# Performance work log

Hardware: AMD Instinct MI355X
Metric: run time of the kernel (lower is better)

## Reference

```python
import jax, jax.numpy as jnp
import numpy as np

B, T, S = 64, 100, 1024
IN, SRC, TRG = 256, 256, 512
ENC = 2 * SRC  # bidirectional encoder hidden width


def setup_inputs() -> dict:
    key = jax.random.key(0)
    ks = jax.random.split(key, 16)
    n = lambda k, shape, sc: jax.random.normal(k, shape, jnp.float32) * sc
    return {
        "idx": 0,
        "input_": n(ks[0], (B, T, IN), 1.0),
        "h0": n(ks[1], (B, TRG), 1.0),
        "c0": n(ks[2], (B, TRG), 1.0),
        "h_attn": jnp.zeros((B, TRG), jnp.float32),
        "encoder_hy": n(ks[3], (B, S, ENC), 1.0),
        "past_attn": jnp.zeros((B, S), jnp.float32),
        "past_dehy": jnp.zeros((B, 1, TRG), jnp.float32),
        # LSTMCell params (PyTorch layout, gate order i,f,g,o)
        "w_ih": n(ks[4], (4 * TRG, IN + TRG), 0.05),
        "b_ih": jnp.zeros((4 * TRG,), jnp.float32),
        "w_hh": n(ks[5], (4 * TRG, TRG), 0.05),
        "b_hh": jnp.zeros((4 * TRG,), jnp.float32),
        # AttentionEncoder luong_concat params
        "w_en": n(ks[6], (TRG, ENC), 0.05),
        "b_en": jnp.zeros((TRG,), jnp.float32),
        "w_de": n(ks[7], (TRG, TRG), 0.05),
        "w_cv": n(ks[8], (TRG, 1), 0.05),
        "w_warp": n(ks[9], (1, TRG), 0.05),
        # attn_out: Linear(ENC + TRG, TRG)
        "w_ao": n(ks[10], (TRG, ENC + TRG), 0.05),
        "b_ao": jnp.zeros((TRG,), jnp.float32),
        # pt_out: Linear(IN + ENC + TRG, 1)
        "w_pt": n(ks[11], (1, IN + ENC + TRG), 0.05),
        "b_pt": jnp.zeros((1,), jnp.float32),
    }


def reference(idx, input_, h0, c0, h_attn, encoder_hy, past_attn, past_dehy,
              w_ih, b_ih, w_hh, b_hh, w_en, b_en, w_de, w_cv, w_warp,
              w_ao, b_ao, w_pt, b_pt):
    # Config: lstm, luong_concat attention, repetition='asee' (coverage),
    # pointer_net=True, attn_decoder=False.
    enc_proj = jnp.einsum('bse,he->bsh', encoder_hy, w_en) + b_en  # hoisted W_en*enhy, [B,S,TRG]
    cv_w = w_cv[:, 0]      # [TRG]
    warp_w = w_warp[0]     # [TRG]
    xs = jnp.swapaxes(input_, 0, 1)  # [T,B,IN]

    def step(carry, x_t):
        h, c, ha, pa = carry
        # LSTMCell on cat(x_t, h_attn)
        x = jnp.concatenate([x_t, ha], axis=1)
        gates = x @ w_ih.T + b_ih + h @ w_hh.T + b_hh
        i, f, g, o = jnp.split(gates, 4, axis=1)
        c_new = jax.nn.sigmoid(f) * c + jax.nn.sigmoid(i) * jnp.tanh(g)
        h_new = jax.nn.sigmoid(o) * jnp.tanh(c_new)
        # luong_concat score with asee coverage term
        agg = jnp.tanh(enc_proj + (h_new @ w_de.T)[:, None, :] + pa[:, :, None] * cv_w)
        attn_ee = jnp.einsum('bsh,h->bs', agg, warp_w)
        attn = jax.nn.softmax(attn_ee, axis=1)
        c_enc = jnp.einsum('bs,bse->be', attn, encoder_hy)  # encoder context
        ha_new = jnp.concatenate([c_enc, h_new], axis=1) @ w_ao.T + b_ao
        pa_new = pa + attn  # coverage accumulation (repetition 'asee')
        p = jax.nn.sigmoid(jnp.concatenate([x_t, h_new, c_enc], axis=1) @ w_pt.T + b_pt)[:, 0]
        return (h_new, c_new, ha_new, pa_new), (ha_new, attn, p)

    (hT, cT, haT, paT), (outs, attns, pgens) = jax.lax.scan(
        step, (h0, c0, h_attn, past_attn), xs)
    output_ = jnp.swapaxes(outs, 0, 1)   # [B,T,TRG]
    p_gen = jnp.swapaxes(pgens, 0, 1)    # [B,T]
    loss_cv = jnp.zeros((1,), jnp.float32)  # only nonzero for 'asee_train'
    # matches original return signature; out_attn kept [T,B,S] as in source
    return (output_, (hT, cT), haT, attns, paT, p_gen, past_dehy, loss_cv)
```

## Files before the change

### kernel.cpp

```cpp
#include <hip/hip_runtime.h>
#include <stdint.h>

typedef __attribute__((ext_vector_type(8))) short short8;
typedef __attribute__((ext_vector_type(4))) float f32x4;

#define DEV static __device__ __forceinline__

DEV unsigned short f2bf(float f) {
  union { float f; uint32_t u; } v; v.f = f;
  uint32_t r = (v.u + 0x7fffu + ((v.u >> 16) & 1u)) >> 16;
  return (unsigned short)r;
}
DEV float bf2f(unsigned short h) {
  union { uint32_t u; float f; } v; v.u = ((uint32_t)h) << 16;
  return v.f;
}
DEV float fsigmoid(float x) { return 1.f / (1.f + __expf(-x)); }
DEV float ftanh(float x) {
  float e = __expf(2.f * x);
  return 1.f - 2.f / (e + 1.f);
}

static const size_t O_HT    = 3276800;
static const size_t O_CT    = 3309568;
static const size_t O_HAT   = 3342336;
static const size_t O_ATTNS = 3375104;
static const size_t O_PAT   = 9928704;
static const size_t O_PGEN  = 9994240;
static const size_t O_PDEHY = 10000640;
static const size_t O_LOSS  = 10033408;

__global__ __launch_bounds__(256) void k_conv_bf16(const float* __restrict__ in,
                                                   unsigned short* __restrict__ out) {
  size_t i = (size_t)blockIdx.x * blockDim.x + threadIdx.x;
  f32x4 v = ((const f32x4*)in)[i];
  uint32_t lo = (uint32_t)f2bf(v[0]) | ((uint32_t)f2bf(v[1]) << 16);
  uint32_t hi = (uint32_t)f2bf(v[2]) | ((uint32_t)f2bf(v[3]) << 16);
  ((uint2*)out)[i] = make_uint2(lo, hi);
}

__global__ __launch_bounds__(256) void k_build_wcomb(const float* __restrict__ wih,
                                                     const float* __restrict__ whh,
                                                     unsigned short* __restrict__ wc) {
  int i = blockIdx.x * blockDim.x + threadIdx.x;
  int base = i * 4;
  int n = base / 1280, k = base - n * 1280;
  const float* src = (k < 768) ? (wih + (size_t)n * 768 + k) : (whh + (size_t)n * 512 + (k - 768));
  f32x4 v = *(const f32x4*)src;
  uint32_t lo = (uint32_t)f2bf(v[0]) | ((uint32_t)f2bf(v[1]) << 16);
  uint32_t hi = (uint32_t)f2bf(v[2]) | ((uint32_t)f2bf(v[3]) << 16);
  ((uint2*)wc)[i] = make_uint2(lo, hi);
}

__global__ __launch_bounds__(256) void k_bias(const float* __restrict__ a,
                                              const float* __restrict__ b,
                                              float* __restrict__ o) {
  int i = blockIdx.x * blockDim.x + threadIdx.x;
  o[i] = a[i] + b[i];
}

template <int MT, int NT, int KK, int OUTBF>
__global__ __launch_bounds__(256) void k_gemm_bt(const unsigned short* __restrict__ A,
                                                 const unsigned short* __restrict__ Bm,
                                                 const float* __restrict__ bias,
                                                 void* __restrict__ C, int ldc) {
  int wid = (int)((blockIdx.x * blockDim.x + threadIdx.x) >> 6);
  int lane = threadIdx.x & 63;
  int tm = wid % MT, tn = wid / MT;
  int r = lane & 15, q = lane >> 4;
  const short8* Ap = (const short8*)(A + (size_t)(tm * 16 + r) * KK + q * 8);
  const short8* Bp = (const short8*)(Bm + (size_t)(tn * 16 + r) * KK + q * 8);
  f32x4 acc = {0.f, 0.f, 0.f, 0.f};
#pragma unroll 4
  for (int kk = 0; kk < KK / 32; ++kk) {
    acc = __builtin_amdgcn_mfma_f32_16x16x32_bf16(Ap[kk * 4], Bp[kk * 4], acc, 0, 0, 0);
  }
  int col = tn * 16 + r;
  float bv = bias ? bias[col] : 0.f;
#pragma unroll
  for (int rg = 0; rg < 4; ++rg) {
    int row = tm * 16 + q * 4 + rg;
    float v = acc[rg] + bv;
    if (OUTBF) ((unsigned short*)C)[(size_t)row * ldc + col] = f2bf(v);
    else       ((float*)C)[(size_t)row * ldc + col] = v;
  }
}

__global__ __launch_bounds__(256) void k_gemm_ha(const float* __restrict__ cenc,
                                                 const unsigned short* __restrict__ hb,
                                                 const unsigned short* __restrict__ Bm,
                                                 const float* __restrict__ bias,
                                                 float* __restrict__ out) {
  int wid = (int)((blockIdx.x * blockDim.x + threadIdx.x) >> 6);
  int lane = threadIdx.x & 63;
  int tm = wid & 3, tn = wid >> 2;
  int r = lane & 15, q = lane >> 4;
  int arow = tm * 16 + r;
  f32x4 acc = {0.f, 0.f, 0.f, 0.f};
#pragma unroll
  for (int kk = 0; kk < 32; ++kk) {
    int k0 = kk * 32 + q * 8;
    short8 a;
    if (k0 < 512) {
      const f32x4* p = (const f32x4*)(cenc + (size_t)arow * 512 + k0);
      f32x4 lo = p[0], hi = p[1];
#pragma unroll
      for (int j = 0; j < 4; ++j) { a[j] = (short)f2bf(lo[j]); a[4 + j] = (short)f2bf(hi[j]); }
    } else {
      a = *(const short8*)(hb + (size_t)arow * 512 + (k0 - 512));
    }
    short8 b = *(const short8*)(Bm + (size_t)(tn * 16 + r) * 1024 + k0);
    acc = __builtin_amdgcn_mfma_f32_16x16x32_bf16(a, b, acc, 0, 0, 0);
  }
  int col = tn * 16 + r;
  float bv = bias[col];
#pragma unroll
  for (int rg = 0; rg < 4; ++rg) {
    int row = tm * 16 + q * 4 + rg;
    out[(size_t)row * 512 + col] = acc[rg] + bv;
  }
}

__global__ __launch_bounds__(256) void k_pack(const float* __restrict__ input_,
                                              const float* __restrict__ ha,
                                              const float* __restrict__ h,
                                              unsigned short* __restrict__ xf, int t) {
  int idx = blockIdx.x * blockDim.x + threadIdx.x;
  int b = idx / 1280, k = idx - b * 1280;
  float v;
  if (k < 256)      v = input_[((size_t)b * 100 + t) * 256 + k];
  else if (k < 768) v = ha[b * 512 + (k - 256)];
  else              v = h[b * 512 + (k - 768)];
  xf[idx] = f2bf(v);
}

__global__ __launch_bounds__(256) void k_lstm(const float* __restrict__ gates,
                                              float* __restrict__ h, float* __restrict__ c,
                                              unsigned short* __restrict__ hb) {
  int idx = blockIdx.x * blockDim.x + threadIdx.x;
  int b = idx >> 9, n = idx & 511;
  const float* g = gates + (size_t)b * 2048;
  float iv = fsigmoid(g[n]);
  float fv = fsigmoid(g[512 + n]);
  float gv = ftanh(g[1024 + n]);
  float ov = fsigmoid(g[1536 + n]);
  float cn = fv * c[idx] + iv * gv;
  float hn = ov * ftanh(cn);
  c[idx] = cn; h[idx] = hn; hb[idx] = f2bf(hn);
}

__global__ __launch_bounds__(256) void k_attn_ee(const unsigned short* __restrict__ ep,
                                                 const float* __restrict__ de,
                                                 const float* __restrict__ cv,
                                                 const float* __restrict__ wwarp,
                                                 const float* __restrict__ pa,
                                                 float* __restrict__ ee) {
  int wid = (int)((blockIdx.x * blockDim.x + threadIdx.x) >> 6);
  int lane = threadIdx.x & 63;
  int b = wid >> 10, s = wid & 1023;
  float pav = pa[(size_t)b * 1024 + s];
  short8 v = *(const short8*)(ep + ((size_t)b * 1024 + s) * 512 + lane * 8);
  const f32x4* dp = (const f32x4*)(de + b * 512 + lane * 8);
  f32x4 d0 = dp[0], d1 = dp[1];
  const f32x4* cp = (const f32x4*)(cv + lane * 8);
  f32x4 c0 = cp[0], c1 = cp[1];
  const f32x4* wp = (const f32x4*)(wwarp + lane * 8);
  f32x4 w0 = wp[0], w1 = wp[1];
  float acc = 0.f;
#pragma unroll
  for (int j = 0; j < 4; ++j) {
    float x0 = bf2f((unsigned short)v[j]) + d0[j] + pav * c0[j];
    acc += ftanh(x0) * w0[j];
    float x1 = bf2f((unsigned short)v[4 + j]) + d1[j] + pav * c1[j];
    acc += ftanh(x1) * w1[j];
  }
#pragma unroll
  for (int off = 32; off > 0; off >>= 1) acc += __shfl_xor(acc, off, 64);
  if (lane == 0) ee[(size_t)b * 1024 + s] = acc;
}

__global__ __launch_bounds__(256) void k_softmax(const float* __restrict__ ee,
                                                 float* __restrict__ attn,
                                                 float* __restrict__ attns_out,
                                                 float* __restrict__ pa,
                                                 float* __restrict__ cenc) {
  int b = blockIdx.x, tid = threadIdx.x;
  int wv = tid >> 6, lane = tid & 63;
  __shared__ float red[4];
  f32x4 v = ((const f32x4*)(ee + (size_t)b * 1024))[tid];
  float m = fmaxf(fmaxf(v[0], v[1]), fmaxf(v[2], v[3]));
#pragma unroll
  for (int off = 32; off > 0; off >>= 1) m = fmaxf(m, __shfl_xor(m, off, 64));
  if (lane == 0) red[wv] = m;
  __syncthreads();
  m = fmaxf(fmaxf(red[0], red[1]), fmaxf(red[2], red[3]));
  f32x4 e;
  e[0] = __expf(v[0] - m); e[1] = __expf(v[1] - m);
  e[2] = __expf(v[2] - m); e[3] = __expf(v[3] - m);
  float s = e[0] + e[1] + e[2] + e[3];
#pragma unroll
  for (int off = 32; off > 0; off >>= 1) s += __shfl_xor(s, off, 64);
  __syncthreads();
  if (lane == 0) red[wv] = s;
  __syncthreads();
  s = red[0] + red[1] + red[2] + red[3];
  float inv = 1.f / s;
  f32x4 a;
  a[0] = e[0] * inv; a[1] = e[1] * inv; a[2] = e[2] * inv; a[3] = e[3] * inv;
  ((f32x4*)(attn + (size_t)b * 1024))[tid] = a;
  ((f32x4*)(attns_out + (size_t)b * 1024))[tid] = a;
  f32x4* pap = (f32x4*)(pa + (size_t)b * 1024);
  f32x4 p = pap[tid];
  p[0] += a[0]; p[1] += a[1]; p[2] += a[2]; p[3] += a[3];
  pap[tid] = p;
  cenc[(size_t)b * 512 + tid] = 0.f;
  cenc[(size_t)b * 512 + 256 + tid] = 0.f;
}

__global__ __launch_bounds__(256) void k_cenc(const float* __restrict__ attn,
                                              const unsigned short* __restrict__ encb,
                                              float* __restrict__ cenc) {
  int b = blockIdx.x >> 2, sq = blockIdx.x & 3;
  int e0 = threadIdx.x * 2;
  const float* at = attn + (size_t)b * 1024 + sq * 256;
  const uint32_t* ep = (const uint32_t*)(encb + ((size_t)b * 1024 + sq * 256) * 512 + e0);
  float a0 = 0.f, a1 = 0.f;
#pragma unroll 4
  for (int s = 0; s < 256; ++s) {
    float w = at[s];
    uint32_t pk = ep[(size_t)s * 256];
    a0 += w * bf2f((unsigned short)(pk & 0xffffu));
    a1 += w * bf2f((unsigned short)(pk >> 16));
  }
  atomicAdd(&cenc[(size_t)b * 512 + e0], a0);
  atomicAdd(&cenc[(size_t)b * 512 + e0 + 1], a1);
}

__global__ __launch_bounds__(256) void k_pout(const float* __restrict__ input_,
                                              const float* __restrict__ h,
                                              const float* __restrict__ c,
                                              const float* __restrict__ cenc,
                                              const float* __restrict__ ha,
                                              const float* __restrict__ wpt,
                                              const float* __restrict__ bpt,
                                              float* __restrict__ dout, int t) {
  int b = blockIdx.x, tid = threadIdx.x;
  float acc = 0.f;
#pragma unroll
  for (int k = tid; k < 1280; k += 256) {
    float x;
    if (k < 256)      x = input_[((size_t)b * 100 + t) * 256 + k];
    else if (k < 768) x = h[(size_t)b * 512 + (k - 256)];
    else              x = cenc[(size_t)b * 512 + (k - 768)];
    acc += x * wpt[k];
  }
  int wv = tid >> 6, lane = tid & 63;
  __shared__ float red[4];
#pragma unroll
  for (int off = 32; off > 0; off >>= 1) acc += __shfl_xor(acc, off, 64);
  if (lane == 0) red[wv] = acc;
  __syncthreads();
  if (tid == 0) {
    float p = fsigmoid(red[0] + red[1] + red[2] + red[3] + bpt[0]);
    dout[O_PGEN + (size_t)b * 100 + t] = p;
  }
  float v0 = ha[(size_t)b * 512 + tid];
  float v1 = ha[(size_t)b * 512 + 256 + tid];
  dout[((size_t)b * 100 + t) * 512 + tid] = v0;
  dout[((size_t)b * 100 + t) * 512 + 256 + tid] = v1;
  if (t == 99) {
    dout[O_HT  + (size_t)b * 512 + tid]       = h[(size_t)b * 512 + tid];
    dout[O_HT  + (size_t)b * 512 + 256 + tid] = h[(size_t)b * 512 + 256 + tid];
    dout[O_CT  + (size_t)b * 512 + tid]       = c[(size_t)b * 512 + tid];
    dout[O_CT  + (size_t)b * 512 + 256 + tid] = c[(size_t)b * 512 + 256 + tid];
    dout[O_HAT + (size_t)b * 512 + tid]       = v0;
    dout[O_HAT + (size_t)b * 512 + 256 + tid] = v1;
  }
}

extern "C" void kernel_launch(void* const* d_in, const int* in_sizes, int n_in,
                              void* d_out, int out_size, void* d_ws, size_t ws_size,
                              hipStream_t stream) {
  const float* input_    = (const float*)d_in[1];
  const float* h0        = (const float*)d_in[2];
  const float* c0        = (const float*)d_in[3];
  const float* h_attn    = (const float*)d_in[4];
  const float* encoder_hy= (const float*)d_in[5];
  const float* past_attn = (const float*)d_in[6];
  const float* past_dehy = (const float*)d_in[7];
  const float* w_ih      = (const float*)d_in[8];
  const float* b_ih      = (const float*)d_in[9];
  const float* w_hh      = (const float*)d_in[10];
  const float* b_hh      = (const float*)d_in[11];
  const float* w_en      = (const float*)d_in[12];
  const float* b_en      = (const float*)d_in[13];
  const float* w_de      = (const float*)d_in[14];
  const float* w_cv      = (const float*)d_in[15];
  const float* w_warp    = (const float*)d_in[16];
  const float* w_ao      = (const float*)d_in[17];
  const float* b_ao      = (const float*)d_in[18];
  const float* w_pt      = (const float*)d_in[19];
  const float* b_pt      = (const float*)d_in[20];

  char* ws = (char*)d_ws;
  unsigned short* encb  = (unsigned short*)(ws + 0);
  unsigned short* epb   = (unsigned short*)(ws + 67108864);
  unsigned short* wcomb = (unsigned short*)(ws + 134217728);
  unsigned short* wenb  = (unsigned short*)(ws + 139460608);
  unsigned short* wdeb  = (unsigned short*)(ws + 139984896);
  unsigned short* waob  = (unsigned short*)(ws + 140509184);
  float* biasc          = (float*)(ws + 141557760);
  unsigned short* xf    = (unsigned short*)(ws + 141565952);
  float* gates          = (float*)(ws + 141729792);
  float* h              = (float*)(ws + 142254080);
  float* c              = (float*)(ws + 142385152);
  float* ha             = (float*)(ws + 142516224);
  unsigned short* hb    = (unsigned short*)(ws + 142647296);
  float* de             = (float*)(ws + 142712832);
  float* ee             = (float*)(ws + 142843904);
  float* attn           = (float*)(ws + 143106048);
  float* cenc           = (float*)(ws + 143368192);

  float* out = (float*)d_out;
  float* pa = out + O_PAT;

  hipMemcpyAsync(h,  h0,     32768 * 4, hipMemcpyDeviceToDevice, stream);
  hipMemcpyAsync(c,  c0,     32768 * 4, hipMemcpyDeviceToDevice, stream);
  hipMemcpyAsync(ha, h_attn, 32768 * 4, hipMemcpyDeviceToDevice, stream);
  hipMemcpyAsync(pa, past_attn, 65536 * 4, hipMemcpyDeviceToDevice, stream);
  hipMemcpyAsync(out + O_PDEHY, past_dehy, 32768 * 4, hipMemcpyDeviceToDevice, stream);
  hipMemsetAsync(out + O_LOSS, 0, 4, stream);

  k_conv_bf16<<<32768, 256, 0, stream>>>(encoder_hy, encb);
  k_conv_bf16<<<256, 256, 0, stream>>>(w_en, wenb);
  k_conv_bf16<<<256, 256, 0, stream>>>(w_de, wdeb);
  k_conv_bf16<<<512, 256, 0, stream>>>(w_ao, waob);
  k_build_wcomb<<<2560, 256, 0, stream>>>(w_ih, w_hh, wcomb);
  k_bias<<<8, 256, 0, stream>>>(b_ih, b_hh, biasc);

  k_gemm_bt<4096, 32, 512, 1><<<32768, 256, 0, stream>>>(encb, wenb, b_en, epb, 512);

  for (int t = 0; t < 100; ++t) {
    k_pack<<<320, 256, 0, stream>>>(input_, ha, h, xf, t);
    k_gemm_bt<4, 128, 1280, 0><<<128, 256, 0, stream>>>(xf, wcomb, biasc, gates, 2048);
    k_lstm<<<128, 256, 0, stream>>>(gates, h, c, hb);
    k_gemm_bt<4, 32, 512, 0><<<32, 256, 0, stream>>>(hb, wdeb, nullptr, de, 512);
    k_attn_ee<<<16384, 256, 0, stream>>>(epb, de, w_cv, w_warp, pa, ee);
    k_softmax<<<64, 256, 0, stream>>>(ee, attn, out + O_ATTNS + (size_t)t * 65536, pa, cenc);
    k_cenc<<<256, 256, 0, stream>>>(attn, encb, cenc);
    k_gemm_ha<<<32, 256, 0, stream>>>(cenc, hb, waob, b_ao, ha);
    k_pout<<<64, 256, 0, stream>>>(input_, h, c, cenc, ha, w_pt, b_pt, out, t);
  }
}
```

Baseline: 8.984 ms.

## Fuse per-step kernels: gates+LSTM, softmax+context, attn-out+pointer

Per-step launches drop from nine to five. Packing, the gate GEMM and the LSTM cell become one kernel that reads fp32 inputs and converts them to bf16 inline. Each wave computes all four gate tiles for its columns, and h's bf16 copy is double-buffered. Softmax and context accumulation merge into one 1024-thread block per batch using shared-memory partials instead of atomics, and the ha GEMM runs as a block-split kernel alongside the pointer-gate reduction. The intent is to cut launch overhead and intermediate global traffic. In exchange, the gate GEMM runs on only 32 blocks and the context step has only 64 blocks.

```diff
diff --git a/kernel.cpp b/kernel.cpp
--- a/kernel.cpp
+++ b/kernel.cpp
@@ -19,6 +19,12 @@
 DEV float ftanh(float x) {
   float e = __expf(2.f * x);
   return 1.f - 2.f / (e + 1.f);
+}
+DEV short8 pack_bf16x8(f32x4 lo, f32x4 hi) {
+  short8 a;
+#pragma unroll
+  for (int j = 0; j < 4; ++j) { a[j] = (short)f2bf(lo[j]); a[4 + j] = (short)f2bf(hi[j]); }
+  return a;
 }
 
 static const size_t O_HT    = 3276800;
@@ -86,67 +92,56 @@
   }
 }
 
-__global__ __launch_bounds__(256) void k_gemm_ha(const float* __restrict__ cenc,
-                                                 const unsigned short* __restrict__ hb,
-                                                 const unsigned short* __restrict__ Bm,
-                                                 const float* __restrict__ bias,
-                                                 float* __restrict__ out) {
-  int wid = (int)((blockIdx.x * blockDim.x + threadIdx.x) >> 6);
-  int lane = threadIdx.x & 63;
-  int tm = wid & 3, tn = wid >> 2;
+__global__ __launch_bounds__(256) void k_gates_lstm(
+    const float* __restrict__ input_, const float* __restrict__ ha,
+    const unsigned short* __restrict__ hbp,
+    const unsigned short* __restrict__ wcomb,
+    const float* __restrict__ biasc,
+    float* __restrict__ h, float* __restrict__ c,
+    unsigned short* __restrict__ hbn,
+    int t) {
+  int wave = threadIdx.x >> 6, lane = threadIdx.x & 63;
   int r = lane & 15, q = lane >> 4;
-  int arow = tm * 16 + r;
-  f32x4 acc = {0.f, 0.f, 0.f, 0.f};
-#pragma unroll
-  for (int kk = 0; kk < 32; ++kk) {
+  int ns = blockIdx.x;
+  int arow = wave * 16 + r;
+  int bcol = ns * 16 + r;
+  const unsigned short* B0 = wcomb + (size_t)(bcol) * 1280;
+  const unsigned short* B1 = wcomb + (size_t)(512 + bcol) * 1280;
+  const unsigned short* B2 = wcomb + (size_t)(1024 + bcol) * 1280;
+  const unsigned short* B3 = wcomb + (size_t)(1536 + bcol) * 1280;
+  f32x4 acc0 = {0.f,0.f,0.f,0.f}, acc1 = acc0, acc2 = acc0, acc3 = acc0;
+#pragma unroll 4
+  for (int kk = 0; kk < 40; ++kk) {
     int k0 = kk * 32 + q * 8;
     short8 a;
-    if (k0 < 512) {
-      const f32x4* p = (const f32x4*)(cenc + (size_t)arow * 512 + k0);
-      f32x4 lo = p[0], hi = p[1];
-#pragma unroll
-      for (int j = 0; j < 4; ++j) { a[j] = (short)f2bf(lo[j]); a[4 + j] = (short)f2bf(hi[j]); }
+    if (k0 < 256) {
+      const f32x4* p = (const f32x4*)(input_ + ((size_t)arow * 100 + t) * 256 + k0);
+      a = pack_bf16x8(p[0], p[1]);
+    } else if (k0 < 768) {
+      const f32x4* p = (const f32x4*)(ha + (size_t)arow * 512 + (k0 - 256));
+      a = pack_bf16x8(p[0], p[1]);
     } else {
-      a = *(const short8*)(hb + (size_t)arow * 512 + (k0 - 512));
-    }
-    short8 b = *(const short8*)(Bm + (size_t)(tn * 16 + r) * 1024 + k0);
-    acc = __builtin_amdgcn_mfma_f32_16x16x32_bf16(a, b, acc, 0, 0, 0);
-  }
-  int col = tn * 16 + r;
-  float bv = bias[col];
+      a = *(const short8*)(hbp + (size_t)arow * 512 + (k0 - 768));
+    }
+    acc0 = __builtin_amdgcn_mfma_f32_16x16x32_bf16(a, *(const short8*)(B0 + k0), acc0, 0, 0, 0);
+    acc1 = __builtin_amdgcn_mfma_f32_16x16x32_bf16(a, *(const short8*)(B1 + k0), acc1, 0, 0, 0);
+    acc2 = __builtin_amdgcn_mfma_f32_16x16x32_bf16(a, *(const short8*)(B2 + k0), acc2, 0, 0, 0);
+    acc3 = __builtin_amdgcn_mfma_f32_16x16x32_bf16(a, *(const short8*)(B3 + k0), acc3, 0, 0, 0);
+  }
+  int col = ns * 16 + r;
+  float bi = biasc[col], bf = biasc[512 + col], bg = biasc[1024 + col], bo = biasc[1536 + col];
 #pragma unroll
   for (int rg = 0; rg < 4; ++rg) {
-    int row = tm * 16 + q * 4 + rg;
-    out[(size_t)row * 512 + col] = acc[rg] + bv;
-  }
-}
-
-__global__ __launch_bounds__(256) void k_pack(const float* __restrict__ input_,
-                                              const float* __restrict__ ha,
-                                              const float* __restrict__ h,
-                                              unsigned short* __restrict__ xf, int t) {
-  int idx = blockIdx.x * blockDim.x + threadIdx.x;
-  int b = idx / 1280, k = idx - b * 1280;
-  float v;
-  if (k < 256)      v = input_[((size_t)b * 100 + t) * 256 + k];
-  else if (k < 768) v = ha[b * 512 + (k - 256)];
-  else              v = h[b * 512 + (k - 768)];
-  xf[idx] = f2bf(v);
-}
-
-__global__ __launch_bounds__(256) void k_lstm(const float* __restrict__ gates,
-                                              float* __restrict__ h, float* __restrict__ c,
-                                              unsigned short* __restrict__ hb) {
-  int idx = blockIdx.x * blockDim.x + threadIdx.x;
-  int b = idx >> 9, n = idx & 511;
-  const float* g = gates + (size_t)b * 2048;
-  float iv = fsigmoid(g[n]);
-  float fv = fsigmoid(g[512 + n]);
-  float gv = ftanh(g[1024 + n]);
-  float ov = fsigmoid(g[1536 + n]);
-  float cn = fv * c[idx] + iv * gv;
-  float hn = ov * ftanh(cn);
-  c[idx] = cn; h[idx] = hn; hb[idx] = f2bf(hn);
+    int b = wave * 16 + q * 4 + rg;
+    size_t idx = (size_t)b * 512 + col;
+    float iv = fsigmoid(acc0[rg] + bi);
+    float fv = fsigmoid(acc1[rg] + bf);
+    float gv = ftanh(acc2[rg] + bg);
+    float ov = fsigmoid(acc3[rg] + bo);
+    float cn = fv * c[idx] + iv * gv;
+    float hn = ov * ftanh(cn);
+    c[idx] = cn; h[idx] = hn; hbn[idx] = f2bf(hn);
+  }
 }
 
 __global__ __launch_bounds__(256) void k_attn_ee(const unsigned short* __restrict__ ep,
@@ -179,102 +174,121 @@
   if (lane == 0) ee[(size_t)b * 1024 + s] = acc;
 }
 
-__global__ __launch_bounds__(256) void k_softmax(const float* __restrict__ ee,
-                                                 float* __restrict__ attn,
-                                                 float* __restrict__ attns_out,
-                                                 float* __restrict__ pa,
-                                                 float* __restrict__ cenc) {
+__global__ __launch_bounds__(1024) void k_softmax_cenc(
+    const float* __restrict__ ee, const unsigned short* __restrict__ encb,
+    float* __restrict__ attns_out, float* __restrict__ pa, float* __restrict__ cenc) {
   int b = blockIdx.x, tid = threadIdx.x;
   int wv = tid >> 6, lane = tid & 63;
-  __shared__ float red[4];
-  f32x4 v = ((const f32x4*)(ee + (size_t)b * 1024))[tid];
-  float m = fmaxf(fmaxf(v[0], v[1]), fmaxf(v[2], v[3]));
+  __shared__ float red[16];
+  __shared__ float attn_s[1024];
+  __shared__ float part[4][512];
+  float v = ee[(size_t)b * 1024 + tid];
+  float m = v;
 #pragma unroll
   for (int off = 32; off > 0; off >>= 1) m = fmaxf(m, __shfl_xor(m, off, 64));
   if (lane == 0) red[wv] = m;
   __syncthreads();
-  m = fmaxf(fmaxf(red[0], red[1]), fmaxf(red[2], red[3]));
-  f32x4 e;
-  e[0] = __expf(v[0] - m); e[1] = __expf(v[1] - m);
-  e[2] = __expf(v[2] - m); e[3] = __expf(v[3] - m);
-  float s = e[0] + e[1] + e[2] + e[3];
+  m = red[0];
+#pragma unroll
+  for (int i = 1; i < 16; ++i) m = fmaxf(m, red[i]);
+  float e = __expf(v - m);
+  float s = e;
 #pragma unroll
   for (int off = 32; off > 0; off >>= 1) s += __shfl_xor(s, off, 64);
   __syncthreads();
   if (lane == 0) red[wv] = s;
   __syncthreads();
-  s = red[0] + red[1] + red[2] + red[3];
-  float inv = 1.f / s;
-  f32x4 a;
-  a[0] = e[0] * inv; a[1] = e[1] * inv; a[2] = e[2] * inv; a[3] = e[3] * inv;
-  ((f32x4*)(attn + (size_t)b * 1024))[tid] = a;
-  ((f32x4*)(attns_out + (size_t)b * 1024))[tid] = a;
-  f32x4* pap = (f32x4*)(pa + (size_t)b * 1024);
-  f32x4 p = pap[tid];
-  p[0] += a[0]; p[1] += a[1]; p[2] += a[2]; p[3] += a[3];
-  pap[tid] = p;
-  cenc[(size_t)b * 512 + tid] = 0.f;
-  cenc[(size_t)b * 512 + 256 + tid] = 0.f;
-}
-
-__global__ __launch_bounds__(256) void k_cenc(const float* __restrict__ attn,
-                                              const unsigned short* __restrict__ encb,
-                                              float* __restrict__ cenc) {
-  int b = blockIdx.x >> 2, sq = blockIdx.x & 3;
-  int e0 = threadIdx.x * 2;
-  const float* at = attn + (size_t)b * 1024 + sq * 256;
-  const uint32_t* ep = (const uint32_t*)(encb + ((size_t)b * 1024 + sq * 256) * 512 + e0);
+  s = 0.f;
+#pragma unroll
+  for (int i = 0; i < 16; ++i) s += red[i];
+  float a = e * (1.f / s);
+  attn_s[tid] = a;
+  attns_out[(size_t)b * 1024 + tid] = a;
+  pa[(size_t)b * 1024 + tid] += a;
+  __syncthreads();
+  int quarter = tid >> 8, cp = tid & 255;
+  const uint32_t* ep = (const uint32_t*)(encb + ((size_t)b * 1024 + quarter * 256) * 512) + cp;
+  const float* at = attn_s + quarter * 256;
   float a0 = 0.f, a1 = 0.f;
-#pragma unroll 4
-  for (int s = 0; s < 256; ++s) {
-    float w = at[s];
-    uint32_t pk = ep[(size_t)s * 256];
+#pragma unroll 8
+  for (int si = 0; si < 256; ++si) {
+    float w = at[si];
+    uint32_t pk = ep[(size_t)si * 256];
     a0 += w * bf2f((unsigned short)(pk & 0xffffu));
     a1 += w * bf2f((unsigned short)(pk >> 16));
   }
-  atomicAdd(&cenc[(size_t)b * 512 + e0], a0);
-  atomicAdd(&cenc[(size_t)b * 512 + e0 + 1], a1);
-}
-
-__global__ __launch_bounds__(256) void k_pout(const float* __restrict__ input_,
-                                              const float* __restrict__ h,
-                                              const float* __restrict__ c,
-                                              const float* __restrict__ cenc,
-                                              const float* __restrict__ ha,
-                                              const float* __restrict__ wpt,
-                                              const float* __restrict__ bpt,
-                                              float* __restrict__ dout, int t) {
-  int b = blockIdx.x, tid = threadIdx.x;
-  float acc = 0.f;
-#pragma unroll
-  for (int k = tid; k < 1280; k += 256) {
-    float x;
-    if (k < 256)      x = input_[((size_t)b * 100 + t) * 256 + k];
-    else if (k < 768) x = h[(size_t)b * 512 + (k - 256)];
-    else              x = cenc[(size_t)b * 512 + (k - 768)];
-    acc += x * wpt[k];
-  }
-  int wv = tid >> 6, lane = tid & 63;
-  __shared__ float red[4];
-#pragma unroll
-  for (int off = 32; off > 0; off >>= 1) acc += __shfl_xor(acc, off, 64);
-  if (lane == 0) red[wv] = acc;
-  __syncthreads();
-  if (tid == 0) {
-    float p = fsigmoid(red[0] + red[1] + red[2] + red[3] + bpt[0]);
-    dout[O_PGEN + (size_t)b * 100 + t] = p;
-  }
-  float v0 = ha[(size_t)b * 512 + tid];
-  float v1 = ha[(size_t)b * 512 + 256 + tid];
-  dout[((size_t)b * 100 + t) * 512 + tid] = v0;
-  dout[((size_t)b * 100 + t) * 512 + 256 + tid] = v1;
-  if (t == 99) {
-    dout[O_HT  + (size_t)b * 512 + tid]       = h[(size_t)b * 512 + tid];
-    dout[O_HT  + (size_t)b * 512 + 256 + tid] = h[(size_t)b * 512 + 256 + tid];
-    dout[O_CT  + (size_t)b * 512 + tid]       = c[(size_t)b * 512 + tid];
-    dout[O_CT  + (size_t)b * 512 + 256 + tid] = c[(size_t)b * 512 + 256 + tid];
-    dout[O_HAT + (size_t)b * 512 + tid]       = v0;
-    dout[O_HAT + (size_t)b * 512 + 256 + tid] = v1;
+  part[quarter][cp * 2] = a0;
+  part[quarter][cp * 2 + 1] = a1;
+  __syncthreads();
+  if (tid < 512)
+    cenc[(size_t)b * 512 + tid] = part[0][tid] + part[1][tid] + part[2][tid] + part[3][tid];
+}
+
+__global__ __launch_bounds__(256) void k_ha_pout(
+    const float* __restrict__ cenc, const unsigned short* __restrict__ hb,
+    const unsigned short* __restrict__ Bm, const float* __restrict__ bias,
+    float* __restrict__ ha,
+    const float* __restrict__ input_, const float* __restrict__ h,
+    const float* __restrict__ c,
+    const float* __restrict__ wpt, const float* __restrict__ bpt,
+    float* __restrict__ dout, int t) {
+  if (blockIdx.x < 32) {
+    int wid = (int)(blockIdx.x * 4 + (threadIdx.x >> 6));
+    int lane = threadIdx.x & 63;
+    int tm = wid & 3, tn = wid >> 2;
+    int r = lane & 15, q = lane >> 4;
+    int arow = tm * 16 + r;
+    f32x4 acc = {0.f, 0.f, 0.f, 0.f};
+#pragma unroll
+    for (int kk = 0; kk < 32; ++kk) {
+      int k0 = kk * 32 + q * 8;
+      short8 a;
+      if (k0 < 512) {
+        const f32x4* p = (const f32x4*)(cenc + (size_t)arow * 512 + k0);
+        a = pack_bf16x8(p[0], p[1]);
+      } else {
+        a = *(const short8*)(hb + (size_t)arow * 512 + (k0 - 512));
+      }
+      short8 bfr = *(const short8*)(Bm + (size_t)(tn * 16 + r) * 1024 + k0);
+      acc = __builtin_amdgcn_mfma_f32_16x16x32_bf16(a, bfr, acc, 0, 0, 0);
+    }
+    int col = tn * 16 + r;
+    float bv = bias[col];
+#pragma unroll
+    for (int rg = 0; rg < 4; ++rg) {
+      int row = tm * 16 + q * 4 + rg;
+      float v = acc[rg] + bv;
+      ha[(size_t)row * 512 + col] = v;
+      dout[((size_t)row * 100 + t) * 512 + col] = v;
+      if (t == 99) dout[O_HAT + (size_t)row * 512 + col] = v;
+    }
+  } else {
+    int b = blockIdx.x - 32, tid = threadIdx.x;
+    float acc = 0.f;
+#pragma unroll
+    for (int k = tid; k < 1280; k += 256) {
+      float x;
+      if (k < 256)      x = input_[((size_t)b * 100 + t) * 256 + k];
+      else if (k < 768) x = h[(size_t)b * 512 + (k - 256)];
+      else              x = cenc[(size_t)b * 512 + (k - 768)];
+      acc += x * wpt[k];
+    }
+    int wv = tid >> 6, lane = tid & 63;
+    __shared__ float red[4];
+#pragma unroll
+    for (int off = 32; off > 0; off >>= 1) acc += __shfl_xor(acc, off, 64);
+    if (lane == 0) red[wv] = acc;
+    __syncthreads();
+    if (tid == 0) {
+      float p = fsigmoid(red[0] + red[1] + red[2] + red[3] + bpt[0]);
+      dout[O_PGEN + (size_t)b * 100 + t] = p;
+    }
+    if (t == 99) {
+      dout[O_HT + (size_t)b * 512 + tid]       = h[(size_t)b * 512 + tid];
+      dout[O_HT + (size_t)b * 512 + 256 + tid] = h[(size_t)b * 512 + 256 + tid];
+      dout[O_CT + (size_t)b * 512 + tid]       = c[(size_t)b * 512 + tid];
+      dout[O_CT + (size_t)b * 512 + 256 + tid] = c[(size_t)b * 512 + 256 + tid];
+    }
   }
 }
 
@@ -310,16 +324,14 @@
   unsigned short* wdeb  = (unsigned short*)(ws + 139984896);
   unsigned short* waob  = (unsigned short*)(ws + 140509184);
   float* biasc          = (float*)(ws + 141557760);
-  unsigned short* xf    = (unsigned short*)(ws + 141565952);
-  float* gates          = (float*)(ws + 141729792);
-  float* h              = (float*)(ws + 142254080);
-  float* c              = (float*)(ws + 142385152);
-  float* ha             = (float*)(ws + 142516224);
-  unsigned short* hb    = (unsigned short*)(ws + 142647296);
-  float* de             = (float*)(ws + 142712832);
-  float* ee             = (float*)(ws + 142843904);
-  float* attn           = (float*)(ws + 143106048);
-  float* cenc           = (float*)(ws + 143368192);
+  float* h              = (float*)(ws + 141565952);
+  float* c              = (float*)(ws + 141697024);
+  float* ha             = (float*)(ws + 141828096);
+  unsigned short* hbA   = (unsigned short*)(ws + 141959168);
+  unsigned short* hbB   = (unsigned short*)(ws + 142024704);
+  float* de             = (float*)(ws + 142090240);
+  float* ee             = (float*)(ws + 142221312);
+  float* cenc           = (float*)(ws + 142483456);
 
   float* out = (float*)d_out;
   float* pa = out + O_PAT;
@@ -335,20 +347,20 @@
   k_conv_bf16<<<256, 256, 0, stream>>>(w_en, wenb);
   k_conv_bf16<<<256, 256, 0, stream>>>(w_de, wdeb);
   k_conv_bf16<<<512, 256, 0, stream>>>(w_ao, waob);
+  k_conv_bf16<<<32, 256, 0, stream>>>(h0, hbA);
   k_build_wcomb<<<2560, 256, 0, stream>>>(w_ih, w_hh, wcomb);
   k_bias<<<8, 256, 0, stream>>>(b_ih, b_hh, biasc);
 
   k_gemm_bt<4096, 32, 512, 1><<<32768, 256, 0, stream>>>(encb, wenb, b_en, epb, 512);
 
   for (int t = 0; t < 100; ++t) {
-    k_pack<<<320, 256, 0, stream>>>(input_, ha, h, xf, t);
-    k_gemm_bt<4, 128, 1280, 0><<<128, 256, 0, stream>>>(xf, wcomb, biasc, gates, 2048);
-    k_lstm<<<128, 256, 0, stream>>>(gates, h, c, hb);
-    k_gemm_bt<4, 32, 512, 0><<<32, 256, 0, stream>>>(hb, wdeb, nullptr, de, 512);
+    unsigned short* hbp = (t & 1) ? hbB : hbA;
+    unsigned short* hbn = (t & 1) ? hbA : hbB;
+    k_gates_lstm<<<32, 256, 0, stream>>>(input_, ha, hbp, wcomb, biasc, h, c, hbn, t);
+    k_gemm_bt<4, 32, 512, 0><<<32, 256, 0, stream>>>(hbn, wdeb, nullptr, de, 512);
     k_attn_ee<<<16384, 256, 0, stream>>>(epb, de, w_cv, w_warp, pa, ee);
-    k_softmax<<<64, 256, 0, stream>>>(ee, attn, out + O_ATTNS + (size_t)t * 65536, pa, cenc);
-    k_cenc<<<256, 256, 0, stream>>>(attn, encb, cenc);
-    k_gemm_ha<<<32, 256, 0, stream>>>(cenc, hb, waob, b_ao, ha);
-    k_pout<<<64, 256, 0, stream>>>(input_, h, c, cenc, ha, w_pt, b_pt, out, t);
-  }
-}
+    k_softmax_cenc<<<64, 1024, 0, stream>>>(ee, encb, out + O_ATTNS + (size_t)t * 65536, pa, cenc);
+    k_ha_pout<<<96, 256, 0, stream>>>(cenc, hbn, waob, b_ao, ha,
+                                      input_, h, c, w_pt, b_pt, out, t);
+  }
+}
```

New measurement: 10.05 ms. +11.9%, slower.
